# Kernel optimization log

Measured on AMD Instinct MI355X. Metric: run time of the kernel, lower is better.

## Reference

```python
import jax, jax.numpy as jnp
import numpy as np

WIN = 9
PAD = WIN // 2
ALPHA = 0.1
BETA = 0.1
EPS_NCC = 1e-5
EPS_SC = 1e-5


def box_sum(x):
    """All-ones WIN^3 box-filter local sum, stride 1, pad WIN//2.
    Implemented separably (3 1-D convs) -- mathematically identical to the
    original single F.conv3d with a ones [1,1,9,9,9] kernel, far cheaper.
    x: [N, 1, D, H, W]"""
    for axis in range(3):
        kshape = [1, 1, 1, 1, 1]
        kshape[2 + axis] = WIN
        kern = jnp.ones(kshape, x.dtype)
        pad = [(0, 0), (0, 0), (0, 0)]
        pad[axis] = (PAD, PAD)
        x = jax.lax.conv_general_dilated(x, kern, (1, 1, 1), pad)
    return x


def setup_inputs() -> dict:
    key = jax.random.key(0)
    k1, k2, k3, k4, k5 = jax.random.split(key, 5)
    B, T, D, H, W = 1, 4, 128, 128, 128
    image = jax.random.normal(k1, (B, T, D, H, W), jnp.float32)
    mask = jax.random.uniform(k2, (B, T, D, H, W), jnp.float32)
    pred_image = jax.random.normal(k3, (B, T, D, H, W), jnp.float32)
    pred_mask = jax.random.uniform(k4, (B, T, D, H, W), jnp.float32)
    flow = jax.random.normal(k5, (T - 1, B, 3, D, H, W), jnp.float32)
    time_diff = jnp.arange(B * T, dtype=jnp.float32).reshape(B, T)
    return {"image": image, "mask": mask, "pred_image": pred_image,
            "pred_mask": pred_mask, "flow": flow, "time_diff": time_diff}


def reference(image, mask, pred_image, pred_mask, flow, time_diff):
    B, T, D, H, W = image.shape
    win_size = WIN ** 3

    # ---- NCC loss: fixed frame (t=0) vs each predicted frame t=1..T-1 ----
    # Per-t (1 - mean(cc_t)) averaged over T-1 equals 1 - mean over the
    # stacked batch since every cc_t has identical shape.
    I = jnp.broadcast_to(image[:, :1], (B, T - 1, D, H, W)).reshape(B * (T - 1), 1, D, H, W)
    J = pred_image[:, 1:].reshape(B * (T - 1), 1, D, H, W)
    I_sum = box_sum(I)
    J_sum = box_sum(J)
    I2_sum = box_sum(I * I)
    J2_sum = box_sum(J * J)
    IJ_sum = box_sum(I * J)
    u_I = I_sum / win_size
    u_J = J_sum / win_size
    cross = IJ_sum - u_J * I_sum - u_I * J_sum + u_I * u_J * win_size
    I_var = I2_sum - 2 * u_I * I_sum + u_I * u_I * win_size
    J_var = J2_sum - 2 * u_J * J_sum + u_J * u_J * win_size
    cc = cross * cross / (I_var * J_var + EPS_NCC)
    ncc = 1.0 - jnp.mean(cc)

    # ---- gradient (flow smoothness) loss, l2 penalty ----
    # flow: [T-1, B, 3, D, H, W]; per-t means of equal-shaped diffs average
    # to the global mean over the leading t axis.
    dy = jnp.square(jnp.abs(flow[:, :, :, 1:, :, :] - flow[:, :, :, :-1, :, :]))
    dx = jnp.square(jnp.abs(flow[:, :, :, :, 1:, :] - flow[:, :, :, :, :-1, :]))
    dz = jnp.square(jnp.abs(flow[:, :, :, :, :, 1:] - flow[:, :, :, :, :, :-1]))
    grad_loss = (jnp.mean(dx) + jnp.mean(dy) + jnp.mean(dz)) / 3.0

    # ---- temporal volume smoothness constraint ----
    area = jnp.sum(pred_mask, axis=(2, 3, 4)).T  # [T, B]
    area = area / jnp.max(area)
    scs = []
    for i in range(T - 2):
        for j in range(i + 1, T - 1):
            for k in range(j + 1, T):
                lam = (time_diff[:, j] - time_diff[:, i] + EPS_SC) / (
                    time_diff[:, k] - time_diff[:, i] + EPS_SC)
                scs.append(jnp.square(area[j] - area[i] - lam * (area[k] - area[i])))
    sc = jnp.mean(jnp.stack(scs, axis=1))

    return ncc + ALPHA * grad_loss + BETA * sc
```

## Files before the change

kernel.cpp:

```cpp
#include <hip/hip_runtime.h>

#define V3 (128 * 128 * 128)

__device__ __forceinline__ float block_reduce(float v, float* sm) {
#pragma unroll
  for (int off = 32; off > 0; off >>= 1) v += __shfl_down(v, off, 64);
  int lane = threadIdx.x & 63;
  int wid  = threadIdx.x >> 6;
  if (lane == 0) sm[wid] = v;
  __syncthreads();
  float r = 0.f;
  if ((int)threadIdx.x < (int)(blockDim.x >> 6)) r = sm[threadIdx.x];
  if (wid == 0) {
#pragma unroll
    for (int off = 4; off > 0; off >>= 1) r += __shfl_down(r, off, 64);
  }
  __syncthreads();
  return r;
}

__device__ __forceinline__ float4 ldz(const float* __restrict__ p, size_t off,
                                      bool v) {
  const float4 q = *(const float4*)(p + off);
  float4 r;
  r.x = v ? q.x : 0.f; r.y = v ? q.y : 0.f;
  r.z = v ? q.z : 0.f; r.w = v ? q.w : 0.f;
  return r;
}

__global__ __launch_bounds__(256) void area_kernel(const float* __restrict__ pm,
                                                   float* __restrict__ acc) {
  __shared__ float sm[8];
  const int t = blockIdx.y;
  const float* p = pm + (size_t)t * V3;
  const int n4 = V3 / 4;
  float s = 0.f;
  for (int i = blockIdx.x * blockDim.x + threadIdx.x; i < n4;
       i += gridDim.x * blockDim.x) {
    float4 a = *(const float4*)(p + 4 * (size_t)i);
    s += (a.x + a.y) + (a.z + a.w);
  }
  s = block_reduce(s, sm);
  if (threadIdx.x == 0) atomicAdd(acc + t, s);
}

__global__ __launch_bounds__(256) void grad_kernel(const float* __restrict__ fl,
                                                   float* __restrict__ acc) {
  __shared__ float sm[8];
  const int w4 = threadIdx.x & 31;
  const int hl = threadIdx.x >> 5;
  const int h  = blockIdx.x * 8 + hl;
  const int d0 = blockIdx.y * 16;
  const int c  = blockIdx.z;
  const float* p = fl + (size_t)c * V3 + (size_t)h * 128 + w4 * 4;
  const bool hv = (h < 127);

  float s = 0.f;
  float4 cur  = *(const float4*)(p + (size_t)d0 * 16384);
  float4 curh = hv ? *(const float4*)(p + (size_t)d0 * 16384 + 128) : cur;

#pragma unroll
  for (int dd = 0; dd < 16; ++dd) {
    const int d = d0 + dd;
    const bool dv = (d < 127);
    float4 nxt = cur, nxth = curh;
    if (dv) {
      nxt = *(const float4*)(p + (size_t)(d + 1) * 16384);
      if (hv) nxth = *(const float4*)(p + (size_t)(d + 1) * 16384 + 128);
    }
    float x;
    x = cur.y - cur.x; s += x * x;
    x = cur.z - cur.y; s += x * x;
    x = cur.w - cur.z; s += x * x;
    float nx = __shfl_down(cur.x, 1, 64);
    if (w4 != 31) { x = nx - cur.w; s += x * x; }
    if (hv) {
      x = curh.x - cur.x; s += x * x;
      x = curh.y - cur.y; s += x * x;
      x = curh.z - cur.z; s += x * x;
      x = curh.w - cur.w; s += x * x;
    }
    if (dv) {
      x = nxt.x - cur.x; s += x * x;
      x = nxt.y - cur.y; s += x * x;
      x = nxt.z - cur.z; s += x * x;
      x = nxt.w - cur.w; s += x * x;
    }
    cur = nxt; curh = nxth;
  }
  s = block_reduce(s, sm);
  if (threadIdx.x == 0) atomicAdd(acc, s);
}

template <bool WITH_I>
__global__ __launch_bounds__(256) void n1_kernel(const float* __restrict__ I0,
                                                 const float* __restrict__ Jall,
                                                 float* __restrict__ FI,
                                                 float* __restrict__ FJall) {
  constexpr int NF = WITH_I ? 5 : 3;
  __shared__ float sI[2][2][136];
  __shared__ float sJ[2][2][136];
  __shared__ float ring[2][9][NF][128];

  const int tz = blockIdx.z;
  const float* J = Jall + (size_t)tz * V3;
  float* FJ = FJall + (size_t)tz * 3 * (size_t)V3;

  const int w  = threadIdx.x & 127;
  const int dl = threadIdx.x >> 7;
  const int d  = blockIdx.y * 2 + dl;
  const int h0 = blockIdx.x * 8;
  const float* Ib = I0 + (size_t)d * 16384;
  const float* Jb = J  + (size_t)d * 16384;

  if (w < 4) {
    sI[dl][0][w] = 0.f; sI[dl][1][w] = 0.f;
    sJ[dl][0][w] = 0.f; sJ[dl][1][w] = 0.f;
  }
  if (w >= 124) {
    sI[dl][0][w + 8] = 0.f; sI[dl][1][w + 8] = 0.f;
    sJ[dl][0][w + 8] = 0.f; sJ[dl][1][w + 8] = 0.f;
  }
#pragma unroll
  for (int sl = 0; sl < 9; ++sl)
#pragma unroll
    for (int f = 0; f < NF; ++f) ring[dl][sl][f][w] = 0.f;

  auto stage = [&](int hh) {
    if (hh >= 0 && hh < 128) {
      const int b = hh & 1;
      if (w < 32) {
        float4 v = *(const float4*)(Ib + hh * 128 + w * 4);
        *(float4*)&sI[dl][b][4 + w * 4] = v;
      } else if (w < 64) {
        const int l = w - 32;
        float4 v = *(const float4*)(Jb + hh * 128 + l * 4);
        *(float4*)&sJ[dl][b][4 + l * 4] = v;
      }
    }
  };

  float S[NF];
#pragma unroll
  for (int f = 0; f < NF; ++f) S[f] = 0.f;

  stage(h0 - 4);
  int slot = (h0 + 32) % 9;

  for (int hh = h0 - 4; hh < h0 + 12; ++hh) {
    __syncthreads();
    stage(hh + 1);
    const int b = hh & 1;
    const bool valid = (hh >= 0) && (hh < 128);

    float Wn[NF];
#pragma unroll
    for (int f = 0; f < NF; ++f) Wn[f] = 0.f;
    if (valid) {
#pragma unroll
      for (int k = 0; k < 9; ++k) {
        float a = sI[dl][b][w + k];
        float bb = sJ[dl][b][w + k];
        if (WITH_I) {
          Wn[0] += a; Wn[1] += a * a;
          Wn[2] += bb; Wn[3] += bb * bb; Wn[4] += a * bb;
        } else {
          Wn[0] += bb; Wn[1] += bb * bb; Wn[2] += a * bb;
        }
      }
    }

#pragma unroll
    for (int f = 0; f < NF; ++f) {
      float old = ring[dl][slot][f][w];
      ring[dl][slot][f][w] = Wn[f];
      S[f] += Wn[f] - old;
    }
    ++slot; if (slot == 9) slot = 0;

    const int ho = hh - 4;
    if (ho >= h0) {
      size_t base = (size_t)d * 16384 + (size_t)ho * 128 + w;
      if (WITH_I) {
        FI[base]                  = S[0];
        FI[(size_t)V3 + base]     = S[1];
        FJ[base]                  = S[2];
        FJ[(size_t)V3 + base]     = S[3];
        FJ[2 * (size_t)V3 + base] = S[4];
      } else {
        FJ[base]                  = S[0];
        FJ[(size_t)V3 + base]     = S[1];
        FJ[2 * (size_t)V3 + base] = S[2];
      }
    }
  }
}

__global__ __launch_bounds__(256) void n2_kernel(const float* __restrict__ FI,
                                                 const float* __restrict__ FJall,
                                                 float* __restrict__ acc) {
  __shared__ float sm[8];
  const float* FJ = FJall + (size_t)blockIdx.z * 3 * (size_t)V3;
  const int w4 = threadIdx.x & 31;
  const int h  = blockIdx.x * 8 + (threadIdx.x >> 5);
  const int d0 = blockIdx.y * 8;
  const size_t hw = (size_t)h * 128 + w4 * 4;

  const float* P0 = FI;
  const float* P1 = FI + (size_t)V3;
  const float* P2 = FJ;
  const float* P3 = FJ + (size_t)V3;
  const float* P4 = FJ + 2 * (size_t)V3;

  float4 S0 = {0,0,0,0}, S1 = {0,0,0,0}, S2 = {0,0,0,0},
         S3 = {0,0,0,0}, S4 = {0,0,0,0};
#pragma unroll
  for (int k = 0; k < 9; ++k) {
    int dd = d0 - 4 + k;
    bool v = (dd >= 0) && (dd < 128);
    size_t a = (size_t)(v ? dd : 0) * 16384 + hw;
    float4 q;
    q = ldz(P0, a, v); S0.x += q.x; S0.y += q.y; S0.z += q.z; S0.w += q.w;
    q = ldz(P1, a, v); S1.x += q.x; S1.y += q.y; S1.z += q.z; S1.w += q.w;
    q = ldz(P2, a, v); S2.x += q.x; S2.y += q.y; S2.z += q.z; S2.w += q.w;
    q = ldz(P3, a, v); S3.x += q.x; S3.y += q.y; S3.z += q.z; S3.w += q.w;
    q = ldz(P4, a, v); S4.x += q.x; S4.y += q.y; S4.z += q.z; S4.w += q.w;
  }

  const float inv_win = 1.0f / 729.0f;
  float accv = 0.f;
#pragma unroll
  for (int dd = 0; dd < 8; ++dd) {
    const int d = d0 + dd;
    {
      float c0, iv, jv;
      c0 = S4.x - S0.x * S2.x * inv_win;
      iv = S1.x - S0.x * S0.x * inv_win;
      jv = S3.x - S2.x * S2.x * inv_win;
      accv += c0 * c0 * __builtin_amdgcn_rcpf(iv * jv + 1e-5f);
      c0 = S4.y - S0.y * S2.y * inv_win;
      iv = S1.y - S0.y * S0.y * inv_win;
      jv = S3.y - S2.y * S2.y * inv_win;
      accv += c0 * c0 * __builtin_amdgcn_rcpf(iv * jv + 1e-5f);
      c0 = S4.z - S0.z * S2.z * inv_win;
      iv = S1.z - S0.z * S0.z * inv_win;
      jv = S3.z - S2.z * S2.z * inv_win;
      accv += c0 * c0 * __builtin_amdgcn_rcpf(iv * jv + 1e-5f);
      c0 = S4.w - S0.w * S2.w * inv_win;
      iv = S1.w - S0.w * S0.w * inv_win;
      jv = S3.w - S2.w * S2.w * inv_win;
      accv += c0 * c0 * __builtin_amdgcn_rcpf(iv * jv + 1e-5f);
    }
    const int da = d + 5, ds = d - 4;
    const bool va = da < 128, vs = ds >= 0;
    const size_t aa = (size_t)(va ? da : 0) * 16384 + hw;
    const size_t as = (size_t)(vs ? ds : 0) * 16384 + hw;
    float4 q, r;
    q = ldz(P0, aa, va); r = ldz(P0, as, vs);
    S0.x += q.x - r.x; S0.y += q.y - r.y; S0.z += q.z - r.z; S0.w += q.w - r.w;
    q = ldz(P1, aa, va); r = ldz(P1, as, vs);
    S1.x += q.x - r.x; S1.y += q.y - r.y; S1.z += q.z - r.z; S1.w += q.w - r.w;
    q = ldz(P2, aa, va); r = ldz(P2, as, vs);
    S2.x += q.x - r.x; S2.y += q.y - r.y; S2.z += q.z - r.z; S2.w += q.w - r.w;
    q = ldz(P3, aa, va); r = ldz(P3, as, vs);
    S3.x += q.x - r.x; S3.y += q.y - r.y; S3.z += q.z - r.z; S3.w += q.w - r.w;
    q = ldz(P4, aa, va); r = ldz(P4, as, vs);
    S4.x += q.x - r.x; S4.y += q.y - r.y; S4.z += q.z - r.z; S4.w += q.w - r.w;
  }

  accv = block_reduce(accv, sm);
  if (threadIdx.x == 0) atomicAdd(acc, accv);
}

__global__ void final_kernel(const float* __restrict__ ws,
                             const float* __restrict__ td,
                             float* __restrict__ out) {
  if (threadIdx.x != 0 || blockIdx.x != 0) return;
  float area[4];
  float amax = -1e30f;
#pragma unroll
  for (int t = 0; t < 4; ++t) {
    area[t] = ws[t];
    amax = fmaxf(amax, area[t]);
  }
  float a[4];
#pragma unroll
  for (int t = 0; t < 4; ++t) a[t] = area[t] / amax;

  float sc = 0.f;
  int cnt = 0;
  for (int i = 0; i < 2; ++i)
    for (int j = i + 1; j < 3; ++j)
      for (int k = j + 1; k < 4; ++k) {
        float lam = (td[j] - td[i] + 1e-5f) / (td[k] - td[i] + 1e-5f);
        float e = a[j] - a[i] - lam * (a[k] - a[i]);
        sc += e * e;
        ++cnt;
      }
  sc /= (float)cnt;

  float ncc  = 1.0f - ws[7] / (3.0f * (float)V3);
  float grad = ws[4] / (3.0f * 9.0f * 127.0f * 128.0f * 128.0f);
  out[0] = ncc + 0.1f * grad + 0.1f * sc;
}

extern "C" void kernel_launch(void* const* d_in, const int* in_sizes, int n_in,
                              void* d_out, int out_size, void* d_ws, size_t ws_size,
                              hipStream_t stream) {
  const float* image      = (const float*)d_in[0];
  const float* pred_image = (const float*)d_in[2];
  const float* pred_mask  = (const float*)d_in[3];
  const float* flow       = (const float*)d_in[4];
  const float* time_diff  = (const float*)d_in[5];
  float* out = (float*)d_out;
  float* wsf = (float*)d_ws;
  float* FI  = wsf + 64;
  float* FJ  = FI + 2 * (size_t)V3;

  hipMemsetAsync(d_ws, 0, 256, stream);

  hipLaunchKernelGGL(area_kernel, dim3(512, 4), dim3(256), 0, stream,
                     pred_mask, wsf);
  hipLaunchKernelGGL(grad_kernel, dim3(16, 8, 9), dim3(256), 0, stream,
                     flow, wsf + 4);

  const size_t need_fused = (64 + 11 * (size_t)V3) * sizeof(float);
  if (ws_size >= need_fused) {
    hipLaunchKernelGGL((n1_kernel<true>), dim3(16, 64, 1), dim3(256), 0, stream,
                       image, pred_image + (size_t)V3, FI, FJ);
    hipLaunchKernelGGL((n1_kernel<false>), dim3(16, 64, 2), dim3(256), 0, stream,
                       image, pred_image + 2 * (size_t)V3, FI,
                       FJ + 3 * (size_t)V3);
    hipLaunchKernelGGL(n2_kernel, dim3(16, 16, 3), dim3(256), 0, stream,
                       FI, FJ, wsf + 7);
  } else {
    for (int t = 0; t < 3; ++t) {
      const float* J = pred_image + (size_t)(t + 1) * V3;
      if (t == 0) {
        hipLaunchKernelGGL((n1_kernel<true>), dim3(16, 64, 1), dim3(256), 0,
                           stream, image, J, FI, FJ);
      } else {
        hipLaunchKernelGGL((n1_kernel<false>), dim3(16, 64, 1), dim3(256), 0,
                           stream, image, J, FI, FJ);
      }
      hipLaunchKernelGGL(n2_kernel, dim3(16, 16, 1), dim3(256), 0, stream,
                         FI, FJ, wsf + 7);
    }
  }

  hipLaunchKernelGGL(final_kernel, dim3(1), dim3(1), 0, stream,
                     wsf, time_diff, out);
}
```

Baseline: 157.8 us.

## Widen n1 h-tile and rework n2 depth sum into direct 12-slice accumulation

n1 now covers 16 rows per block instead of 8, halving the grid and cutting the 8-row halo overhead of the separable box filter. n2 drops the sliding-window add/subtract over 8 depth outputs. Each block now handles 4 outputs, loading 12 slices once and adding each slice into every window that contains it. This removes the subtract loads and the serial dependency but re-reads more halo (12 loads per 4 outputs instead of 25 per 8) and keeps 80 float accumulators in registers, with a launch bound of 2 blocks.

Result: faster. 153.9 us (-2.5%).

```diff
diff --git a/kernel.cpp b/kernel.cpp
--- a/kernel.cpp
+++ b/kernel.cpp
@@ -26,6 +26,19 @@
   r.x = v ? q.x : 0.f; r.y = v ? q.y : 0.f;
   r.z = v ? q.z : 0.f; r.w = v ? q.w : 0.f;
   return r;
+}
+
+__device__ __forceinline__ void add4(float4& a, const float4 b) {
+  a.x += b.x; a.y += b.y; a.z += b.z; a.w += b.w;
+}
+
+__device__ __forceinline__ float ccf(float i, float i2, float j, float j2,
+                                     float ij) {
+  const float inv_win = 1.0f / 729.0f;
+  float cross = ij - i * j * inv_win;
+  float iv    = i2 - i * i * inv_win;
+  float jv    = j2 - j * j * inv_win;
+  return cross * cross * __builtin_amdgcn_rcpf(iv * jv + 1e-5f);
 }
 
 __global__ __launch_bounds__(256) void area_kernel(const float* __restrict__ pm,
@@ -109,7 +122,7 @@
   const int w  = threadIdx.x & 127;
   const int dl = threadIdx.x >> 7;
   const int d  = blockIdx.y * 2 + dl;
-  const int h0 = blockIdx.x * 8;
+  const int h0 = blockIdx.x * 16;
   const float* Ib = I0 + (size_t)d * 16384;
   const float* Jb = J  + (size_t)d * 16384;
 
@@ -147,7 +160,7 @@
   stage(h0 - 4);
   int slot = (h0 + 32) % 9;
 
-  for (int hh = h0 - 4; hh < h0 + 12; ++hh) {
+  for (int hh = h0 - 4; hh < h0 + 20; ++hh) {
     __syncthreads();
     stage(hh + 1);
     const int b = hh & 1;
@@ -196,14 +209,14 @@
   }
 }
 
-__global__ __launch_bounds__(256) void n2_kernel(const float* __restrict__ FI,
-                                                 const float* __restrict__ FJall,
-                                                 float* __restrict__ acc) {
+__global__ __launch_bounds__(256, 2) void n2_kernel(const float* __restrict__ FI,
+                                                    const float* __restrict__ FJall,
+                                                    float* __restrict__ acc) {
   __shared__ float sm[8];
   const float* FJ = FJall + (size_t)blockIdx.z * 3 * (size_t)V3;
   const int w4 = threadIdx.x & 31;
   const int h  = blockIdx.x * 8 + (threadIdx.x >> 5);
-  const int d0 = blockIdx.y * 8;
+  const int d0 = blockIdx.y * 4;
   const size_t hw = (size_t)h * 128 + w4 * 4;
 
   const float* P0 = FI;
@@ -212,60 +225,41 @@
   const float* P3 = FJ + (size_t)V3;
   const float* P4 = FJ + 2 * (size_t)V3;
 
-  float4 S0 = {0,0,0,0}, S1 = {0,0,0,0}, S2 = {0,0,0,0},
-         S3 = {0,0,0,0}, S4 = {0,0,0,0};
-#pragma unroll
-  for (int k = 0; k < 9; ++k) {
-    int dd = d0 - 4 + k;
-    bool v = (dd >= 0) && (dd < 128);
-    size_t a = (size_t)(v ? dd : 0) * 16384 + hw;
-    float4 q;
-    q = ldz(P0, a, v); S0.x += q.x; S0.y += q.y; S0.z += q.z; S0.w += q.w;
-    q = ldz(P1, a, v); S1.x += q.x; S1.y += q.y; S1.z += q.z; S1.w += q.w;
-    q = ldz(P2, a, v); S2.x += q.x; S2.y += q.y; S2.z += q.z; S2.w += q.w;
-    q = ldz(P3, a, v); S3.x += q.x; S3.y += q.y; S3.z += q.z; S3.w += q.w;
-    q = ldz(P4, a, v); S4.x += q.x; S4.y += q.y; S4.z += q.z; S4.w += q.w;
-  }
-
-  const float inv_win = 1.0f / 729.0f;
+  float4 S[4][5];
+#pragma unroll
+  for (int o = 0; o < 4; ++o)
+#pragma unroll
+    for (int f = 0; f < 5; ++f) S[o][f] = make_float4(0.f, 0.f, 0.f, 0.f);
+
+#pragma unroll
+  for (int k = 0; k < 12; ++k) {
+    const int sidx = d0 - 4 + k;
+    const bool v = (sidx >= 0) && (sidx < 128);
+    const size_t a = (size_t)(v ? sidx : 0) * 16384 + hw;
+    float4 q0 = ldz(P0, a, v);
+    float4 q1 = ldz(P1, a, v);
+    float4 q2 = ldz(P2, a, v);
+    float4 q3 = ldz(P3, a, v);
+    float4 q4 = ldz(P4, a, v);
+#pragma unroll
+    for (int o = 0; o < 4; ++o) {
+      if (o <= k && k <= o + 8) {
+        add4(S[o][0], q0);
+        add4(S[o][1], q1);
+        add4(S[o][2], q2);
+        add4(S[o][3], q3);
+        add4(S[o][4], q4);
+      }
+    }
+  }
+
   float accv = 0.f;
 #pragma unroll
-  for (int dd = 0; dd < 8; ++dd) {
-    const int d = d0 + dd;
-    {
-      float c0, iv, jv;
-      c0 = S4.x - S0.x * S2.x * inv_win;
-      iv = S1.x - S0.x * S0.x * inv_win;
-      jv = S3.x - S2.x * S2.x * inv_win;
-      accv += c0 * c0 * __builtin_amdgcn_rcpf(iv * jv + 1e-5f);
-      c0 = S4.y - S0.y * S2.y * inv_win;
-      iv = S1.y - S0.y * S0.y * inv_win;
-      jv = S3.y - S2.y * S2.y * inv_win;
-      accv += c0 * c0 * __builtin_amdgcn_rcpf(iv * jv + 1e-5f);
-      c0 = S4.z - S0.z * S2.z * inv_win;
-      iv = S1.z - S0.z * S0.z * inv_win;
-      jv = S3.z - S2.z * S2.z * inv_win;
-      accv += c0 * c0 * __builtin_amdgcn_rcpf(iv * jv + 1e-5f);
-      c0 = S4.w - S0.w * S2.w * inv_win;
-      iv = S1.w - S0.w * S0.w * inv_win;
-      jv = S3.w - S2.w * S2.w * inv_win;
-      accv += c0 * c0 * __builtin_amdgcn_rcpf(iv * jv + 1e-5f);
-    }
-    const int da = d + 5, ds = d - 4;
-    const bool va = da < 128, vs = ds >= 0;
-    const size_t aa = (size_t)(va ? da : 0) * 16384 + hw;
-    const size_t as = (size_t)(vs ? ds : 0) * 16384 + hw;
-    float4 q, r;
-    q = ldz(P0, aa, va); r = ldz(P0, as, vs);
-    S0.x += q.x - r.x; S0.y += q.y - r.y; S0.z += q.z - r.z; S0.w += q.w - r.w;
-    q = ldz(P1, aa, va); r = ldz(P1, as, vs);
-    S1.x += q.x - r.x; S1.y += q.y - r.y; S1.z += q.z - r.z; S1.w += q.w - r.w;
-    q = ldz(P2, aa, va); r = ldz(P2, as, vs);
-    S2.x += q.x - r.x; S2.y += q.y - r.y; S2.z += q.z - r.z; S2.w += q.w - r.w;
-    q = ldz(P3, aa, va); r = ldz(P3, as, vs);
-    S3.x += q.x - r.x; S3.y += q.y - r.y; S3.z += q.z - r.z; S3.w += q.w - r.w;
-    q = ldz(P4, aa, va); r = ldz(P4, as, vs);
-    S4.x += q.x - r.x; S4.y += q.y - r.y; S4.z += q.z - r.z; S4.w += q.w - r.w;
+  for (int o = 0; o < 4; ++o) {
+    accv += ccf(S[o][0].x, S[o][1].x, S[o][2].x, S[o][3].x, S[o][4].x);
+    accv += ccf(S[o][0].y, S[o][1].y, S[o][2].y, S[o][3].y, S[o][4].y);
+    accv += ccf(S[o][0].z, S[o][1].z, S[o][2].z, S[o][3].z, S[o][4].z);
+    accv += ccf(S[o][0].w, S[o][1].w, S[o][2].w, S[o][3].w, S[o][4].w);
   }
 
   accv = block_reduce(accv, sm);
@@ -326,24 +320,24 @@
 
   const size_t need_fused = (64 + 11 * (size_t)V3) * sizeof(float);
   if (ws_size >= need_fused) {
-    hipLaunchKernelGGL((n1_kernel<true>), dim3(16, 64, 1), dim3(256), 0, stream,
+    hipLaunchKernelGGL((n1_kernel<true>), dim3(8, 64, 1), dim3(256), 0, stream,
                        image, pred_image + (size_t)V3, FI, FJ);
-    hipLaunchKernelGGL((n1_kernel<false>), dim3(16, 64, 2), dim3(256), 0, stream,
+    hipLaunchKernelGGL((n1_kernel<false>), dim3(8, 64, 2), dim3(256), 0, stream,
                        image, pred_image + 2 * (size_t)V3, FI,
                        FJ + 3 * (size_t)V3);
-    hipLaunchKernelGGL(n2_kernel, dim3(16, 16, 3), dim3(256), 0, stream,
+    hipLaunchKernelGGL(n2_kernel, dim3(16, 32, 3), dim3(256), 0, stream,
                        FI, FJ, wsf + 7);
   } else {
     for (int t = 0; t < 3; ++t) {
       const float* J = pred_image + (size_t)(t + 1) * V3;
       if (t == 0) {
-        hipLaunchKernelGGL((n1_kernel<true>), dim3(16, 64, 1), dim3(256), 0,
+        hipLaunchKernelGGL((n1_kernel<true>), dim3(8, 64, 1), dim3(256), 0,
                            stream, image, J, FI, FJ);
       } else {
-        hipLaunchKernelGGL((n1_kernel<false>), dim3(16, 64, 1), dim3(256), 0,
+        hipLaunchKernelGGL((n1_kernel<false>), dim3(8, 64, 1), dim3(256), 0,
                            stream, image, J, FI, FJ);
       }
-      hipLaunchKernelGGL(n2_kernel, dim3(16, 16, 1), dim3(256), 0, stream,
+      hipLaunchKernelGGL(n2_kernel, dim3(16, 32, 1), dim3(256), 0, stream,
                          FI, FJ, wsf + 7);
     }
   }
```
